# Kernel tuning notes

Hardware: AMD Instinct MI355X
Metric: run time of the kernel (lower is better)

The kernel has to match this reference:

```python
import jax, jax.numpy as jnp
import numpy as np

N_NODES = 100000
N_EDGES = 1600000
IN_CH = 128
HID = 64
HEADS = 4
N_GRAPHS = 64
NEG_SLOPE = 0.2
LN_EPS = 1e-5


def setup_inputs() -> dict:
    key = jax.random.key(0)
    ks = jax.random.split(key, 24)
    C1 = HID // HEADS  # 16 per-head channels for conv1
    inp = {
        "x": jax.random.normal(ks[0], (N_NODES, IN_CH), dtype=jnp.float32),
        "edge_index": jax.random.randint(ks[1], (2, N_EDGES), 0, N_NODES, dtype=jnp.int64),
        "batch": jnp.sort(jax.random.randint(ks[2], (N_NODES,), 0, N_GRAPHS, dtype=jnp.int64)),
        "num_graphs": N_GRAPHS,
        # conv1: GATConv(IN_CH -> C1, heads=HEADS, concat)
        "W1": jax.random.normal(ks[3], (IN_CH, HEADS * C1), dtype=jnp.float32) * 0.05,
        "att_src1": jax.random.normal(ks[4], (HEADS, C1), dtype=jnp.float32) * 0.1,
        "att_dst1": jax.random.normal(ks[5], (HEADS, C1), dtype=jnp.float32) * 0.1,
        "b1": jnp.zeros((HEADS * C1,), dtype=jnp.float32),
        # conv2: GATConv(HID -> HID, heads=1)
        "W2": jax.random.normal(ks[6], (HID, HID), dtype=jnp.float32) * 0.1,
        "att_src2": jax.random.normal(ks[7], (1, HID), dtype=jnp.float32) * 0.1,
        "att_dst2": jax.random.normal(ks[8], (1, HID), dtype=jnp.float32) * 0.1,
        "b2": jnp.zeros((HID,), dtype=jnp.float32),
        "ln_g": jnp.ones((HID,), dtype=jnp.float32),
        "ln_b": jnp.zeros((HID,), dtype=jnp.float32),
        "w_pool": jax.random.normal(ks[9], (HID, 1), dtype=jnp.float32) * 0.1,
        "b_pool": jnp.zeros((1,), dtype=jnp.float32),
        "w_fc1": jax.random.normal(ks[10], (HID, HID), dtype=jnp.float32) * 0.1,
        "b_fc1": jnp.zeros((HID,), dtype=jnp.float32),
        "w_fc2": jax.random.normal(ks[11], (HID, 1), dtype=jnp.float32) * 0.1,
        "b_fc2": jnp.zeros((1,), dtype=jnp.float32),
    }
    return inp


def gat_conv(x, src, dst, n_nodes, W, att_src, att_dst, bias, heads, out_ch):
    """PyG GATConv (add_self_loops already folded into src/dst)."""
    h = (x @ W).reshape(n_nodes, heads, out_ch)         # [N,H,C]
    a_s = jnp.sum(h * att_src[None], axis=-1)           # [N,H]
    a_d = jnp.sum(h * att_dst[None], axis=-1)           # [N,H]
    alpha = jax.nn.leaky_relu(a_s[src] + a_d[dst], NEG_SLOPE)  # [E,H]
    amax = jax.ops.segment_max(alpha, dst, num_segments=n_nodes)
    amax = jnp.where(jnp.isfinite(amax), amax, 0.0)
    ex = jnp.exp(alpha - amax[dst])
    denom = jax.ops.segment_sum(ex, dst, num_segments=n_nodes)
    w = ex / (denom[dst] + 1e-16)                       # segment softmax over in-edges
    msg = h[src] * w[:, :, None]                        # [E,H,C]
    out = jax.ops.segment_sum(msg, dst, num_segments=n_nodes)
    return out.reshape(n_nodes, heads * out_ch) + bias


def reference(x, edge_index, batch, num_graphs, W1, att_src1, att_dst1, b1,
              W2, att_src2, att_dst2, b2, ln_g, ln_b, w_pool, b_pool,
              w_fc1, b_fc1, w_fc2, b_fc2):
    n = x.shape[0]
    loop = jnp.arange(n, dtype=edge_index.dtype)
    src = jnp.concatenate([edge_index[0], loop])
    dst = jnp.concatenate([edge_index[1], loop])

    h = gat_conv(x, src, dst, n, W1, att_src1, att_dst1, b1, HEADS, HID // HEADS)
    h = jax.nn.elu(h)                                   # dropout is identity in eval
    h_res = h
    h = gat_conv(h, src, dst, n, W2, att_src2, att_dst2, b2, 1, HID)
    h = h + h_res
    mu = jnp.mean(h, axis=-1, keepdims=True)
    var = jnp.mean(jnp.square(h - mu), axis=-1, keepdims=True)
    h = (h - mu) / jnp.sqrt(var + LN_EPS) * ln_g + ln_b
    h = jax.nn.elu(h)

    attn = jax.nn.softmax(h @ w_pool + b_pool, axis=0)  # softmax over ALL nodes (dim=0)
    pooled = jax.ops.segment_sum(h * attn, batch, num_segments=num_graphs)  # [G,HID]
    z = jax.nn.elu(pooled @ w_fc1 + b_fc1)
    return z @ w_fc2 + b_fc2                            # [G,1]
```

## Files before the change

kernel.cpp:

```cpp
#include <hip/hip_runtime.h>
#include <math.h>

#define NN 100000
#define NE 1600000
#define ICH 128
#define HID 64
#define NGR 64
#define NB_SCAN 391

__device__ __forceinline__ float lrelu(float x){ return x > 0.f ? x : 0.2f*x; }
__device__ __forceinline__ float eluf(float x){ return x > 0.f ? x : expm1f(x); }

__device__ __forceinline__ float bf2f(unsigned short u){
  return __uint_as_float(((unsigned int)u) << 16);
}
__device__ __forceinline__ unsigned short f2bf(float f){
  unsigned int u = __float_as_uint(f);
  return (unsigned short)((u + 0x7FFF + ((u >> 16) & 1)) >> 16);
}

__device__ __forceinline__ float wsum64(float v){
  #pragma unroll
  for (int m = 32; m >= 1; m >>= 1) v += __shfl_xor(v, m);
  return v;
}
__device__ __forceinline__ float wsum16(float v){
  v += __shfl_xor(v, 8); v += __shfl_xor(v, 4);
  v += __shfl_xor(v, 2); v += __shfl_xor(v, 1);
  return v;
}
__device__ __forceinline__ int wscan_incl(int v){
  const int lane = threadIdx.x & 63;
  #pragma unroll
  for (int d = 1; d < 64; d <<= 1){
    int t = __shfl_up(v, d);
    if (lane >= d) v += t;
  }
  return v;
}

__global__ __launch_bounds__(256) void k_deg(const int* __restrict__ ei_dst,
                                             int* __restrict__ deg)
{
  const int lo = (blockIdx.x & 3) * 25000, hi = lo + 25000;
  const int nb = gridDim.x >> 2, ib = blockIdx.x >> 2;
  for (int e = ib * 256 + threadIdx.x; e < NE; e += nb * 256){
    int d = ei_dst[e];
    if (d >= lo && d < hi) atomicAdd(&deg[d], 1);
  }
}

__global__ __launch_bounds__(256) void k_scanA(const int* __restrict__ deg,
    int* __restrict__ rowptr, int* __restrict__ bsum)
{
  int i = blockIdx.x * 256 + threadIdx.x;
  int v = (i < NN) ? deg[i] : 0;
  int incl = wscan_incl(v);
  __shared__ int wsums[4];
  int w = threadIdx.x >> 6, lane = threadIdx.x & 63;
  if (lane == 63) wsums[w] = incl;
  __syncthreads();
  int off = 0;
  for (int k = 0; k < w; ++k) off += wsums[k];
  if (i < NN) rowptr[i] = incl - v + off;
  if (threadIdx.x == 255) bsum[blockIdx.x] = off + incl;
}

__global__ __launch_bounds__(512) void k_scanB(const int* __restrict__ bsum,
                                               int* __restrict__ boff)
{
  int i = threadIdx.x;
  int v = (i < NB_SCAN) ? bsum[i] : 0;
  int incl = wscan_incl(v);
  __shared__ int wsums[8];
  int w = threadIdx.x >> 6, lane = threadIdx.x & 63;
  if (lane == 63) wsums[w] = incl;
  __syncthreads();
  int off = 0;
  for (int k = 0; k < w; ++k) off += wsums[k];
  if (i < NB_SCAN) boff[i] = incl - v + off;
}

__global__ __launch_bounds__(256) void k_scanC(int* __restrict__ rowptr,
    const int* __restrict__ boff, int* __restrict__ cursor)
{
  int i = blockIdx.x * 256 + threadIdx.x;
  if (i < NN){
    int val = rowptr[i] + boff[blockIdx.x];
    rowptr[i] = val;
    cursor[i] = val;
  }
  if (i == 0) rowptr[NN] = NE;
}

__global__ __launch_bounds__(256) void k_scatter(const int* __restrict__ ei,
    int* __restrict__ cursor, int* __restrict__ csr_src)
{
  const int lo = (blockIdx.x & 7) * 12500, hi = lo + 12500;
  const int nb = gridDim.x >> 3, ib = blockIdx.x >> 3;
  for (int e = ib * 256 + threadIdx.x; e < NE; e += nb * 256){
    int d = ei[NE + e];
    if (d >= lo && d < hi){
      int pos = atomicAdd(&cursor[d], 1);
      csr_src[pos] = ei[e];
    }
  }
}

__global__ __launch_bounds__(256) void k_gemm1(const float* __restrict__ x,
    const float* __restrict__ W1, const float* __restrict__ asw,
    const float* __restrict__ adw, unsigned short* __restrict__ h1b,
    float* __restrict__ as1, float* __restrict__ ad1)
{
  __shared__ float xs[16 * ICH];
  const int t = threadIdx.x;
  const int n0 = blockIdx.x * 16;
  const float4* xg4 = (const float4*)(x + (size_t)n0 * ICH);
  float4* xs4 = (float4*)xs;
  xs4[t]       = xg4[t];
  xs4[t + 256] = xg4[t + 256];
  __syncthreads();

  const int lane = t & 63;
  const float* xr = xs + (t >> 6) * 4 * ICH;
  float a0 = 0.f, a1 = 0.f, a2 = 0.f, a3 = 0.f;
  #pragma unroll 8
  for (int k = 0; k < ICH; ++k){
    const float w = W1[k * HID + lane];
    a0 = fmaf(xr[k],          w, a0);
    a1 = fmaf(xr[ICH + k],    w, a1);
    a2 = fmaf(xr[2*ICH + k],  w, a2);
    a3 = fmaf(xr[3*ICH + k],  w, a3);
  }
  const float sw = asw[lane], dw = adw[lane];
  const int nw = n0 + (t >> 6) * 4;
  float acc[4] = {a0, a1, a2, a3};
  #pragma unroll
  for (int i = 0; i < 4; ++i){
    const int n = nw + i;
    h1b[(size_t)n * HID + lane] = f2bf(acc[i]);
    float ps = wsum16(acc[i] * sw);
    float pd = wsum16(acc[i] * dw);
    if ((lane & 15) == 0){
      as1[n * 4 + (lane >> 4)] = ps;
      ad1[n * 4 + (lane >> 4)] = pd;
    }
  }
}

__global__ __launch_bounds__(256) void k_conv1(const int* __restrict__ rowptr,
    const int* __restrict__ csr_src, const float* __restrict__ as1,
    const float* __restrict__ ad1, const unsigned short* __restrict__ h1b,
    const float* __restrict__ b1, float* __restrict__ hb)
{
  __shared__ float2 buf[256];
  const int t = threadIdx.x;
  const int lane = t & 63;
  const int h = lane >> 4;
  const int m = lane & 15;
  const int woff = t & 192;
  const int n = (blockIdx.x * 256 + t) >> 6;
  const int row0 = __builtin_amdgcn_readfirstlane(rowptr[n]);
  const int row1 = __builtin_amdgcn_readfirstlane(rowptr[n + 1]);
  const float adh = ad1[4 * n + h];
  const float eself = __expf(lrelu(as1[4 * n + h] + adh));
  const unsigned short* __restrict__ hrow = h1b + lane;
  float a0 = eself * bf2f(hrow[(unsigned)n << 6]);
  float a1 = 0.f, a2 = 0.f, a3 = 0.f;
  float den_p = 0.f;
  const int rbase = woff + (lane & 48);
  for (int base = row0; base < row1; base += 16){
    const int cnt = min(16, row1 - base);
    int s = 0; float e = 0.f;
    if (m < cnt){
      s = csr_src[base + m];
      e = __expf(lrelu(as1[4 * s + h] + adh));
    }
    den_p += e;
    buf[woff + lane] = make_float2(e, __int_as_float(s));
    int j = 0;
    for (; j + 4 <= cnt; j += 4){
      float2 p0 = buf[rbase + j];
      float2 p1 = buf[rbase + j + 1];
      float2 p2 = buf[rbase + j + 2];
      float2 p3 = buf[rbase + j + 3];
      float v0 = bf2f(hrow[(unsigned)__float_as_int(p0.y) << 6]);
      float v1 = bf2f(hrow[(unsigned)__float_as_int(p1.y) << 6]);
      float v2 = bf2f(hrow[(unsigned)__float_as_int(p2.y) << 6]);
      float v3 = bf2f(hrow[(unsigned)__float_as_int(p3.y) << 6]);
      a0 = fmaf(v0, p0.x, a0);
      a1 = fmaf(v1, p1.x, a1);
      a2 = fmaf(v2, p2.x, a2);
      a3 = fmaf(v3, p3.x, a3);
    }
    for (; j < cnt; ++j){
      float2 p0 = buf[rbase + j];
      a0 = fmaf(bf2f(hrow[(unsigned)__float_as_int(p0.y) << 6]), p0.x, a0);
    }
  }
  float acc = (a0 + a1) + (a2 + a3);
  float den = wsum16(den_p) + eself;
  float o = acc / (den + 1e-16f) + b1[lane];
  hb[((size_t)n << 6) | lane] = eluf(o);
}

__global__ __launch_bounds__(256) void k_gemm2(const float* __restrict__ h,
    const float* __restrict__ W2, const float* __restrict__ asw,
    const float* __restrict__ adw, unsigned short* __restrict__ h2b,
    float* __restrict__ as2, float* __restrict__ ad2)
{
  __shared__ float hs[16 * HID];
  const int t = threadIdx.x;
  const int n0 = blockIdx.x * 16;
  const float4* hg4 = (const float4*)(h + (size_t)n0 * HID);
  float4* hs4 = (float4*)hs;
  hs4[t] = hg4[t];
  __syncthreads();

  const int lane = t & 63;
  const float* hr = hs + (t >> 6) * 4 * HID;
  float a0 = 0.f, a1 = 0.f, a2 = 0.f, a3 = 0.f;
  #pragma unroll 8
  for (int k = 0; k < HID; ++k){
    const float w = W2[k * HID + lane];
    a0 = fmaf(hr[k],          w, a0);
    a1 = fmaf(hr[HID + k],    w, a1);
    a2 = fmaf(hr[2*HID + k],  w, a2);
    a3 = fmaf(hr[3*HID + k],  w, a3);
  }
  const float sw = asw[lane], dw = adw[lane];
  const int nw = n0 + (t >> 6) * 4;
  float acc[4] = {a0, a1, a2, a3};
  #pragma unroll
  for (int i = 0; i < 4; ++i){
    const int n = nw + i;
    h2b[(size_t)n * HID + lane] = f2bf(acc[i]);
    float ps = wsum64(acc[i] * sw);
    float pd = wsum64(acc[i] * dw);
    if (lane == 0){ as2[n] = ps; ad2[n] = pd; }
  }
}

__global__ __launch_bounds__(256) void k_conv2(const int* __restrict__ rowptr,
    const int* __restrict__ csr_src, const float* __restrict__ as2,
    const float* __restrict__ ad2, const unsigned short* __restrict__ h2b,
    const float* __restrict__ b2, float* __restrict__ hb,
    const float* __restrict__ lng, const float* __restrict__ lnb,
    const float* __restrict__ wpool, const float* __restrict__ bpool,
    float* __restrict__ es)
{
  __shared__ float2 buf[256];
  const int t = threadIdx.x;
  const int lane = t & 63;
  const int woff = t & 192;
  const int n = (blockIdx.x * 256 + t) >> 6;
  const int row0 = __builtin_amdgcn_readfirstlane(rowptr[n]);
  const int row1 = __builtin_amdgcn_readfirstlane(rowptr[n + 1]);
  const float adn = ad2[n];
  const float eself = __expf(lrelu(as2[n] + adn));
  const unsigned short* __restrict__ hrow = h2b + lane;
  float a0 = eself * bf2f(hrow[(unsigned)n << 6]);
  float a1 = 0.f, a2 = 0.f, a3 = 0.f;
  float den_p = 0.f;
  for (int base = row0; base < row1; base += 64){
    const int cnt = min(64, row1 - base);
    int s = 0; float e = 0.f;
    if (lane < cnt){
      s = csr_src[base + lane];
      e = __expf(lrelu(as2[s] + adn));
    }
    den_p += e;
    buf[woff + lane] = make_float2(e, __int_as_float(s));
    int j = 0;
    for (; j + 4 <= cnt; j += 4){
      float2 p0 = buf[woff + j];
      float2 p1 = buf[woff + j + 1];
      float2 p2 = buf[woff + j + 2];
      float2 p3 = buf[woff + j + 3];
      float v0 = bf2f(hrow[(unsigned)__float_as_int(p0.y) << 6]);
      float v1 = bf2f(hrow[(unsigned)__float_as_int(p1.y) << 6]);
      float v2 = bf2f(hrow[(unsigned)__float_as_int(p2.y) << 6]);
      float v3 = bf2f(hrow[(unsigned)__float_as_int(p3.y) << 6]);
      a0 = fmaf(v0, p0.x, a0);
      a1 = fmaf(v1, p1.x, a1);
      a2 = fmaf(v2, p2.x, a2);
      a3 = fmaf(v3, p3.x, a3);
    }
    for (; j < cnt; ++j){
      float2 p0 = buf[woff + j];
      a0 = fmaf(bf2f(hrow[(unsigned)__float_as_int(p0.y) << 6]), p0.x, a0);
    }
  }
  float acc = (a0 + a1) + (a2 + a3);
  float den = wsum64(den_p) + eself;
  const size_t idxn = ((size_t)n << 6) | lane;
  float tv = acc / (den + 1e-16f) + b2[lane] + hb[idxn];
  float mu  = wsum64(tv) * (1.f / 64.f);
  float dv  = tv - mu;
  float var = wsum64(dv * dv) * (1.f / 64.f);
  float hv = dv * (1.f / sqrtf(var + 1e-5f)) * lng[lane] + lnb[lane];
  hv = eluf(hv);
  hb[idxn] = hv;
  float sl = wsum64(hv * wpool[lane]) + bpool[0];
  if (lane == 0) es[n] = __expf(sl);
}

__global__ __launch_bounds__(256) void k_sumes(const float* __restrict__ es,
                                               float* __restrict__ S)
{
  float v = 0.f;
  for (int i = blockIdx.x * 256 + threadIdx.x; i < NN; i += gridDim.x * 256)
    v += es[i];
  v = wsum64(v);
  __shared__ float red[4];
  if ((threadIdx.x & 63) == 0) red[threadIdx.x >> 6] = v;
  __syncthreads();
  if (threadIdx.x == 0) atomicAdd(S, red[0] + red[1] + red[2] + red[3]);
}

__global__ __launch_bounds__(256) void k_pool(const float* __restrict__ hf,
    const float* __restrict__ es, const int* __restrict__ batch,
    const float* __restrict__ S, float* __restrict__ pooled)
{
  const int lane = threadIdx.x & 63;
  const int wseg = blockIdx.x * 4 + (threadIdx.x >> 6);
  const int base = wseg * 64;
  if (base >= NN) return;
  const float invS = 1.f / S[0];
  int end = base + 64; if (end > NN) end = NN;
  float acc = 0.f;
  int gprev = batch[base];
  for (int n = base; n < end; ++n){
    int g = batch[n];
    if (g != gprev){
      atomicAdd(&pooled[gprev * HID + lane], acc);
      acc = 0.f; gprev = g;
    }
    acc = fmaf(hf[(size_t)n * HID + lane], es[n] * invS, acc);
  }
  atomicAdd(&pooled[gprev * HID + lane], acc);
}

__global__ __launch_bounds__(64) void k_head(const float* __restrict__ pooled,
    const float* __restrict__ wfc1, const float* __restrict__ bfc1,
    const float* __restrict__ wfc2, const float* __restrict__ bfc2,
    float* __restrict__ out)
{
  const int g = blockIdx.x, j = threadIdx.x;
  const float* pr = pooled + g * HID;
  float acc = bfc1[j];
  #pragma unroll 4
  for (int k = 0; k < HID; ++k) acc = fmaf(pr[k], wfc1[k * HID + j], acc);
  float z = eluf(acc);
  float r = wsum64(z * wfc2[j]);
  if (j == 0) out[g] = r + bfc2[0];
}

extern "C" void kernel_launch(void* const* d_in, const int* in_sizes, int n_in,
                              void* d_out, int out_size, void* d_ws, size_t ws_size,
                              hipStream_t stream)
{
  const float* x     = (const float*)d_in[0];
  const int*   ei    = (const int*)d_in[1];
  const int*   batch = (const int*)d_in[2];
  const float* W1    = (const float*)d_in[4];
  const float* asw1  = (const float*)d_in[5];
  const float* adw1  = (const float*)d_in[6];
  const float* b1    = (const float*)d_in[7];
  const float* W2    = (const float*)d_in[8];
  const float* asw2  = (const float*)d_in[9];
  const float* adw2  = (const float*)d_in[10];
  const float* b2    = (const float*)d_in[11];
  const float* lng   = (const float*)d_in[12];
  const float* lnb   = (const float*)d_in[13];
  const float* wpool = (const float*)d_in[14];
  const float* bpool = (const float*)d_in[15];
  const float* wfc1  = (const float*)d_in[16];
  const float* bfc1  = (const float*)d_in[17];
  const float* wfc2  = (const float*)d_in[18];
  const float* bfc2  = (const float*)d_in[19];

  float* ws = (float*)d_ws;
  float* hb     = ws;
  float* as1    = ws +  6400000;
  float* ad1    = ws +  6800000;
  float* as2    = ws +  7200000;
  float* ad2    = ws +  7300000;
  float* es     = ws +  7400000;
  float* pooled = ws +  7500000;
  float* Ssum   = ws +  7504096;
  unsigned short* hub = (unsigned short*)(ws + 7504100);
  int* iw       = (int*)(ws + 10704100);
  int* rowptr   = iw;
  int* cursor   = iw + 100004;
  int* deg      = iw + 200008;
  int* bsum     = iw + 300008;
  int* boff     = iw + 300520;
  int* csr_src  = iw + 301032;

  hipMemsetAsync(deg, 0, (size_t)NN * 4, stream);
  hipMemsetAsync(pooled, 0, (size_t)NGR * 64 * 4, stream);
  hipMemsetAsync(Ssum, 0, 4, stream);

  k_deg    <<<2048, 256, 0, stream>>>(ei + NE, deg);
  k_scanA  <<<NB_SCAN, 256, 0, stream>>>(deg, rowptr, bsum);
  k_scanB  <<<1, 512, 0, stream>>>(bsum, boff);
  k_scanC  <<<NB_SCAN, 256, 0, stream>>>(rowptr, boff, cursor);
  k_scatter<<<2048, 256, 0, stream>>>(ei, cursor, csr_src);

  k_gemm1<<<6250, 256, 0, stream>>>(x, W1, asw1, adw1, hub, as1, ad1);
  k_conv1<<<25000, 256, 0, stream>>>(rowptr, csr_src, as1, ad1, hub, b1, hb);
  k_gemm2<<<6250, 256, 0, stream>>>(hb, W2, asw2, adw2, hub, as2, ad2);
  k_conv2<<<25000, 256, 0, stream>>>(rowptr, csr_src, as2, ad2, hub, b2, hb,
                                     lng, lnb, wpool, bpool, es);
  k_sumes<<<128, 256, 0, stream>>>(es, Ssum);
  k_pool <<<391, 256, 0, stream>>>(hb, es, batch, Ssum, pooled);
  k_head <<<64, 64, 0, stream>>>(pooled, wfc1, bfc1, wfc2, bfc2, (float*)d_out);
}
```

Before: 403.2 us.

## Fuse conv2 projection into conv1 epilogue and fold softmax sum into pooling

The W2 projection and attention-score computation move into the conv1 aggregation kernel, with W2 staged in shared memory per block, which eliminates the separate gemm2 pass over the hidden features. The global softmax denominator is now accumulated inside the pooling kernel and applied in the head, so the separate reduction kernel is dropped. W1 is also staged in shared memory in gemm1, and the degree-count kernel partitions nodes into eight ranges instead of four. In exchange, every small block reloads the full weight matrix into LDS, which raises LDS use and may lower occupancy in the gather-heavy kernel.

```diff
diff --git a/kernel.cpp b/kernel.cpp
--- a/kernel.cpp
+++ b/kernel.cpp
@@ -42,8 +42,8 @@
 __global__ __launch_bounds__(256) void k_deg(const int* __restrict__ ei_dst,
                                              int* __restrict__ deg)
 {
-  const int lo = (blockIdx.x & 3) * 25000, hi = lo + 25000;
-  const int nb = gridDim.x >> 2, ib = blockIdx.x >> 2;
+  const int lo = (blockIdx.x & 7) * 12500, hi = lo + 12500;
+  const int nb = gridDim.x >> 3, ib = blockIdx.x >> 3;
   for (int e = ib * 256 + threadIdx.x; e < NE; e += nb * 256){
     int d = ei_dst[e];
     if (d >= lo && d < hi) atomicAdd(&deg[d], 1);
@@ -113,12 +113,17 @@
     float* __restrict__ as1, float* __restrict__ ad1)
 {
   __shared__ float xs[16 * ICH];
+  __shared__ float w1s[ICH * HID];
   const int t = threadIdx.x;
   const int n0 = blockIdx.x * 16;
   const float4* xg4 = (const float4*)(x + (size_t)n0 * ICH);
   float4* xs4 = (float4*)xs;
   xs4[t]       = xg4[t];
   xs4[t + 256] = xg4[t + 256];
+  const float4* wg4 = (const float4*)W1;
+  float4* ws4 = (float4*)w1s;
+  #pragma unroll
+  for (int i = 0; i < 8; ++i) ws4[t + 256 * i] = wg4[t + 256 * i];
   __syncthreads();
 
   const int lane = t & 63;
@@ -126,7 +131,7 @@
   float a0 = 0.f, a1 = 0.f, a2 = 0.f, a3 = 0.f;
   #pragma unroll 8
   for (int k = 0; k < ICH; ++k){
-    const float w = W1[k * HID + lane];
+    const float w = w1s[k * HID + lane];
     a0 = fmaf(xr[k],          w, a0);
     a1 = fmaf(xr[ICH + k],    w, a1);
     a2 = fmaf(xr[2*ICH + k],  w, a2);
@@ -148,17 +153,31 @@
   }
 }
 
-__global__ __launch_bounds__(256) void k_conv1(const int* __restrict__ rowptr,
+__global__ __launch_bounds__(256) void k_conv1g2(const int* __restrict__ rowptr,
     const int* __restrict__ csr_src, const float* __restrict__ as1,
     const float* __restrict__ ad1, const unsigned short* __restrict__ h1b,
-    const float* __restrict__ b1, float* __restrict__ hb)
+    const float* __restrict__ b1, float* __restrict__ hb,
+    const float* __restrict__ W2, const float* __restrict__ asw2,
+    const float* __restrict__ adw2, unsigned short* __restrict__ h2b,
+    float* __restrict__ as2, float* __restrict__ ad2)
 {
   __shared__ float2 buf[256];
+  __shared__ float w2s[HID * HID];
+  __shared__ float orow[4][HID];
   const int t = threadIdx.x;
+  {
+    const float4* wg = (const float4*)W2;
+    float4* wsm = (float4*)w2s;
+    #pragma unroll
+    for (int i = 0; i < 4; ++i) wsm[t + 256 * i] = wg[t + 256 * i];
+  }
+  __syncthreads();
+
   const int lane = t & 63;
   const int h = lane >> 4;
   const int m = lane & 15;
   const int woff = t & 192;
+  const int wid = t >> 6;
   const int n = (blockIdx.x * 256 + t) >> 6;
   const int row0 = __builtin_amdgcn_readfirstlane(rowptr[n]);
   const int row1 = __builtin_amdgcn_readfirstlane(rowptr[n + 1]);
@@ -200,45 +219,18 @@
   }
   float acc = (a0 + a1) + (a2 + a3);
   float den = wsum16(den_p) + eself;
-  float o = acc / (den + 1e-16f) + b1[lane];
-  hb[((size_t)n << 6) | lane] = eluf(o);
-}
-
-__global__ __launch_bounds__(256) void k_gemm2(const float* __restrict__ h,
-    const float* __restrict__ W2, const float* __restrict__ asw,
-    const float* __restrict__ adw, unsigned short* __restrict__ h2b,
-    float* __restrict__ as2, float* __restrict__ ad2)
-{
-  __shared__ float hs[16 * HID];
-  const int t = threadIdx.x;
-  const int n0 = blockIdx.x * 16;
-  const float4* hg4 = (const float4*)(h + (size_t)n0 * HID);
-  float4* hs4 = (float4*)hs;
-  hs4[t] = hg4[t];
-  __syncthreads();
-
-  const int lane = t & 63;
-  const float* hr = hs + (t >> 6) * 4 * HID;
-  float a0 = 0.f, a1 = 0.f, a2 = 0.f, a3 = 0.f;
+  float o = eluf(acc / (den + 1e-16f) + b1[lane]);
+  hb[((size_t)n << 6) | lane] = o;
+
+  orow[wid][lane] = o;
+  float g = 0.f;
   #pragma unroll 8
-  for (int k = 0; k < HID; ++k){
-    const float w = W2[k * HID + lane];
-    a0 = fmaf(hr[k],          w, a0);
-    a1 = fmaf(hr[HID + k],    w, a1);
-    a2 = fmaf(hr[2*HID + k],  w, a2);
-    a3 = fmaf(hr[3*HID + k],  w, a3);
-  }
-  const float sw = asw[lane], dw = adw[lane];
-  const int nw = n0 + (t >> 6) * 4;
-  float acc[4] = {a0, a1, a2, a3};
-  #pragma unroll
-  for (int i = 0; i < 4; ++i){
-    const int n = nw + i;
-    h2b[(size_t)n * HID + lane] = f2bf(acc[i]);
-    float ps = wsum64(acc[i] * sw);
-    float pd = wsum64(acc[i] * dw);
-    if (lane == 0){ as2[n] = ps; ad2[n] = pd; }
-  }
+  for (int k = 0; k < HID; ++k)
+    g = fmaf(orow[wid][k], w2s[k * HID + lane], g);
+  h2b[((size_t)n << 6) | lane] = f2bf(g);
+  float ps = wsum64(g * asw2[lane]);
+  float pd = wsum64(g * adw2[lane]);
+  if (lane == 0){ as2[n] = ps; ad2[n] = pd; }
 }
 
 __global__ __launch_bounds__(256) void k_conv2(const int* __restrict__ rowptr,
@@ -305,30 +297,16 @@
   if (lane == 0) es[n] = __expf(sl);
 }
 
-__global__ __launch_bounds__(256) void k_sumes(const float* __restrict__ es,
-                                               float* __restrict__ S)
-{
-  float v = 0.f;
-  for (int i = blockIdx.x * 256 + threadIdx.x; i < NN; i += gridDim.x * 256)
-    v += es[i];
-  v = wsum64(v);
-  __shared__ float red[4];
-  if ((threadIdx.x & 63) == 0) red[threadIdx.x >> 6] = v;
-  __syncthreads();
-  if (threadIdx.x == 0) atomicAdd(S, red[0] + red[1] + red[2] + red[3]);
-}
-
 __global__ __launch_bounds__(256) void k_pool(const float* __restrict__ hf,
     const float* __restrict__ es, const int* __restrict__ batch,
-    const float* __restrict__ S, float* __restrict__ pooled)
+    float* __restrict__ S, float* __restrict__ pooled)
 {
   const int lane = threadIdx.x & 63;
   const int wseg = blockIdx.x * 4 + (threadIdx.x >> 6);
   const int base = wseg * 64;
   if (base >= NN) return;
-  const float invS = 1.f / S[0];
   int end = base + 64; if (end > NN) end = NN;
-  float acc = 0.f;
+  float acc = 0.f, sp = 0.f;
   int gprev = batch[base];
   for (int n = base; n < end; ++n){
     int g = batch[n];
@@ -336,22 +314,26 @@
       atomicAdd(&pooled[gprev * HID + lane], acc);
       acc = 0.f; gprev = g;
     }
-    acc = fmaf(hf[(size_t)n * HID + lane], es[n] * invS, acc);
+    float e = es[n];
+    sp += e;
+    acc = fmaf(hf[(size_t)n * HID + lane], e, acc);
   }
   atomicAdd(&pooled[gprev * HID + lane], acc);
+  if (lane == 0) atomicAdd(S, sp);
 }
 
 __global__ __launch_bounds__(64) void k_head(const float* __restrict__ pooled,
-    const float* __restrict__ wfc1, const float* __restrict__ bfc1,
-    const float* __restrict__ wfc2, const float* __restrict__ bfc2,
-    float* __restrict__ out)
+    const float* __restrict__ S, const float* __restrict__ wfc1,
+    const float* __restrict__ bfc1, const float* __restrict__ wfc2,
+    const float* __restrict__ bfc2, float* __restrict__ out)
 {
   const int g = blockIdx.x, j = threadIdx.x;
+  const float invS = 1.f / S[0];
   const float* pr = pooled + g * HID;
-  float acc = bfc1[j];
+  float acc = 0.f;
   #pragma unroll 4
   for (int k = 0; k < HID; ++k) acc = fmaf(pr[k], wfc1[k * HID + j], acc);
-  float z = eluf(acc);
+  float z = eluf(acc * invS + bfc1[j]);
   float r = wsum64(z * wfc2[j]);
   if (j == 0) out[g] = r + bfc2[0];
 }
@@ -389,8 +371,9 @@
   float* es     = ws +  7400000;
   float* pooled = ws +  7500000;
   float* Ssum   = ws +  7504096;
-  unsigned short* hub = (unsigned short*)(ws + 7504100);
-  int* iw       = (int*)(ws + 10704100);
+  unsigned short* h1b = (unsigned short*)(ws +  7504100);
+  unsigned short* h2b = (unsigned short*)(ws + 10704100);
+  int* iw       = (int*)(ws + 13904100);
   int* rowptr   = iw;
   int* cursor   = iw + 100004;
   int* deg      = iw + 200008;
@@ -408,12 +391,12 @@
   k_scanC  <<<NB_SCAN, 256, 0, stream>>>(rowptr, boff, cursor);
   k_scatter<<<2048, 256, 0, stream>>>(ei, cursor, csr_src);
 
-  k_gemm1<<<6250, 256, 0, stream>>>(x, W1, asw1, adw1, hub, as1, ad1);
-  k_conv1<<<25000, 256, 0, stream>>>(rowptr, csr_src, as1, ad1, hub, b1, hb);
-  k_gemm2<<<6250, 256, 0, stream>>>(hb, W2, asw2, adw2, hub, as2, ad2);
-  k_conv2<<<25000, 256, 0, stream>>>(rowptr, csr_src, as2, ad2, hub, b2, hb,
-                                     lng, lnb, wpool, bpool, es);
-  k_sumes<<<128, 256, 0, stream>>>(es, Ssum);
-  k_pool <<<391, 256, 0, stream>>>(hb, es, batch, Ssum, pooled);
-  k_head <<<64, 64, 0, stream>>>(pooled, wfc1, bfc1, wfc2, bfc2, (float*)d_out);
-}
+  k_gemm1  <<<6250, 256, 0, stream>>>(x, W1, asw1, adw1, h1b, as1, ad1);
+  k_conv1g2<<<25000, 256, 0, stream>>>(rowptr, csr_src, as1, ad1, h1b, b1, hb,
+                                       W2, asw2, adw2, h2b, as2, ad2);
+  k_conv2  <<<25000, 256, 0, stream>>>(rowptr, csr_src, as2, ad2, h2b, b2, hb,
+                                       lng, lnb, wpool, bpool, es);
+  k_pool   <<<391, 256, 0, stream>>>(hb, es, batch, Ssum, pooled);
+  k_head   <<<64, 64, 0, stream>>>(pooled, Ssum, wfc1, bfc1, wfc2, bfc2,
+                                   (float*)d_out);
+}
```

Result: slower. 427.5 us (+6.0%).
